# Optimization experiments

Measured on AMD Instinct MI355X. Metric: run time of the kernel, lower is better.

The kernel has to match this reference:

```python
import jax, jax.numpy as jnp
import numpy as np

TIME_STEP = 0.1  # matches module-level time_step in the torch source
STEPS = 65536


def setup_inputs() -> dict:
    key = jax.random.key(0)
    k1, k2 = jax.random.split(key)
    x = jax.random.normal(k1, (12,), dtype=jnp.float32)          # initial state [pos(6), vel(6)]
    actions = jax.random.normal(k2, (STEPS, 6), dtype=jnp.float32)  # learned per-step accelerations
    return {"x": x, "actions": actions}


def reference(x, actions):
    dt = jnp.float32(TIME_STEP)
    half_dt2 = jnp.float32(0.5) * dt * dt

    def step(state, a):
        # state: [12] = [pos(6), vel(6)]; a: [6]
        pos = state[:6] + state[6:] * dt + half_dt2 * a
        vel = state[6:] + dt * a
        new_state = jnp.concatenate([pos, vel])
        return new_state, new_state

    _, states = jax.lax.scan(step, x, actions)  # states: [steps, 12]
    return (states, actions)
```

## Files before the change

### kernel.cpp

```cpp
#include <hip/hip_runtime.h>


#define STEPS   65536
#define NCH     6
#define STATE   12
#define NB      256
#define CHUNK   (STEPS / NB)
#define BLK     (NCH * 64)
#define ACT_OFF (STEPS * STATE)

__device__ double             g_bsum[NB * NCH * 2];
__device__ unsigned long long g_flag[NB * 8];

__global__ __launch_bounds__(BLK) void k_fused(const float4* __restrict__ act4,
                                               const float* __restrict__ x,
                                               float* __restrict__ out) {
    __shared__ float sIn[CHUNK * NCH];
    __shared__ float sOut[CHUNK * STATE];
    __shared__ unsigned long long sEpoch;
    const int b = blockIdx.x, tid = threadIdx.x;

    float4 v = act4[b * (CHUNK * NCH / 4) + tid];
    ((float4*)sIn)[tid] = v;
    __syncthreads();

    const int c = tid >> 6, lane = tid & 63;

    {
        double sA = 0.0, sW = 0.0;
#pragma unroll
        for (int k = 0; k < 4; ++k) {
            const int   tl = k * 64 + lane;
            const float a  = sIn[tl * NCH + c];
            sA += (double)a;
            sW += (double)(b * CHUNK + tl) * (double)a;
        }
#pragma unroll
        for (int off = 32; off > 0; off >>= 1) {
            sA += __shfl_down(sA, off, 64);
            sW += __shfl_down(sW, off, 64);
        }
        if (lane == 0) {
            __hip_atomic_store(&g_bsum[(b * NCH + c) * 2 + 0], sA,
                               __ATOMIC_RELAXED, __HIP_MEMORY_SCOPE_AGENT);
            __hip_atomic_store(&g_bsum[(b * NCH + c) * 2 + 1], sW,
                               __ATOMIC_RELAXED, __HIP_MEMORY_SCOPE_AGENT);
        }
    }

    __syncthreads();
    if (tid == 0) {
        unsigned long long old = __hip_atomic_fetch_add(&g_flag[b * 8], 1ULL,
                                                        __ATOMIC_RELAXED,
                                                        __HIP_MEMORY_SCOPE_AGENT);
        sEpoch = old + 1ULL;
    }
    __syncthreads();
    const unsigned long long e = sEpoch;
    if (tid < 64) {
        unsigned pend = 0xFu;
        for (;;) {
#pragma unroll
            for (int j = 0; j < 4; ++j) {
                if (pend & (1u << j)) {
                    unsigned long long f =
                        __hip_atomic_load(&g_flag[(lane + 64 * j) * 8],
                                          __ATOMIC_RELAXED,
                                          __HIP_MEMORY_SCOPE_AGENT);
                    if (f >= e) pend &= ~(1u << j);
                }
            }
            if (__all(pend == 0u)) break;
            __builtin_amdgcn_s_sleep(1);
        }
        __builtin_amdgcn_fence(__ATOMIC_ACQUIRE, "agent");
    }
    __syncthreads();

    ((float4*)(out + ACT_OFF))[b * (CHUNK * NCH / 4) + tid] = v;

    double offA, offW;
    {
        const double2* bs2 = (const double2*)g_bsum;
        double vA = 0.0, vW = 0.0;
#pragma unroll
        for (int k = 0; k < 4; ++k) {
            const int idx = k * 64 + lane;
            if (idx < b) {
                const double2 p = bs2[idx * NCH + c];
                vA += p.x;
                vW += p.y;
            }
        }
#pragma unroll
        for (int off = 32; off > 0; off >>= 1) {
            vA += __shfl_down(vA, off, 64);
            vW += __shfl_down(vW, off, 64);
        }
        offA = __shfl(vA, 0, 64);
        offW = __shfl(vW, 0, 64);
    }

    const double dt  = (double)0.1f;
    const double dt2 = dt * dt;
    const double p0  = (double)x[c];
    const double v0  = (double)x[NCH + c];

    double accA = offA, accW = offW;
#pragma unroll
    for (int k = 0; k < 4; ++k) {
        const int   tl = k * 64 + lane;
        const int   t  = b * CHUNK + tl;
        const float a  = sIn[tl * NCH + c];
        double iA = (double)a;
        double iW = (double)t * (double)a;
#pragma unroll
        for (int off = 1; off < 64; off <<= 1) {
            const double uA = __shfl_up(iA, off, 64);
            const double uW = __shfl_up(iW, off, 64);
            if (lane >= off) { iA += uA; iW += uW; }
        }
        const double runA = accA + iA;
        const double runW = accW + iW;
        const double vel = v0 + dt * runA;
        const double pos = p0 + dt * (double)(t + 1) * v0
                         + dt2 * (((double)t + 0.5) * runA - runW);
        sOut[tl * STATE + c]       = (float)pos;
        sOut[tl * STATE + NCH + c] = (float)vel;
        accA += __shfl(iA, 63, 64);
        accW += __shfl(iW, 63, 64);
    }
    __syncthreads();

    const float4* so4 = (const float4*)sOut;
    float4*       o4  = (float4*)out;
    o4[b * (CHUNK * STATE / 4) + tid]       = so4[tid];
    o4[b * (CHUNK * STATE / 4) + BLK + tid] = so4[BLK + tid];
}

extern "C" void kernel_launch(void* const* d_in, const int* in_sizes, int n_in,
                              void* d_out, int out_size, void* d_ws, size_t ws_size,
                              hipStream_t stream) {
    const float*  x    = (const float*)d_in[0];
    const float4* act4 = (const float4*)d_in[1];
    float*        out  = (float*)d_out;

    hipLaunchKernelGGL(k_fused, dim3(NB), dim3(BLK), 0, stream,
                       act4, x, out);
}
```

Baseline: 63.74 us.

## Replace all-to-all flag polling with single-block gather and broadcast go flag

Grid barrier now has block 0 alone poll all per-block flags, then publish a single go counter that every other block spins on. Previously each block polled all 256 flags. The intra-chunk scans, the action copy-out and the x loads move ahead of the wait so they overlap with barrier latency. The flag fetch_add becomes a load plus store, and the barrier adds an extra hop through block 0.

```diff
diff --git a/kernel.cpp b/kernel.cpp
--- a/kernel.cpp
+++ b/kernel.cpp
@@ -11,6 +11,7 @@
 
 __device__ double             g_bsum[NB * NCH * 2];
 __device__ unsigned long long g_flag[NB * 8];
+__device__ unsigned long long g_go;
 
 __global__ __launch_bounds__(BLK) void k_fused(const float4* __restrict__ act4,
                                                const float* __restrict__ x,
@@ -19,12 +20,17 @@
     __shared__ float sOut[CHUNK * STATE];
     __shared__ unsigned long long sEpoch;
     const int b = blockIdx.x, tid = threadIdx.x;
+    const int c = tid >> 6, lane = tid & 63;
 
     float4 v = act4[b * (CHUNK * NCH / 4) + tid];
+    const double p0 = (double)x[c];
+    const double v0 = (double)x[NCH + c];
+    unsigned long long myflag = 0ULL;
+    if (tid == 0)
+        myflag = __hip_atomic_load(&g_flag[b * 8], __ATOMIC_RELAXED,
+                                   __HIP_MEMORY_SCOPE_AGENT);
     ((float4*)sIn)[tid] = v;
     __syncthreads();
-
-    const int c = tid >> 6, lane = tid & 63;
 
     {
         double sA = 0.0, sW = 0.0;
@@ -47,17 +53,16 @@
                                __ATOMIC_RELAXED, __HIP_MEMORY_SCOPE_AGENT);
         }
     }
-
-    __syncthreads();
-    if (tid == 0) {
-        unsigned long long old = __hip_atomic_fetch_add(&g_flag[b * 8], 1ULL,
-                                                        __ATOMIC_RELAXED,
-                                                        __HIP_MEMORY_SCOPE_AGENT);
-        sEpoch = old + 1ULL;
-    }
+    if (tid == 0) sEpoch = myflag + 1ULL;
     __syncthreads();
     const unsigned long long e = sEpoch;
-    if (tid < 64) {
+    if (tid == 0)
+        __hip_atomic_store(&g_flag[b * 8], e,
+                           __ATOMIC_RELAXED, __HIP_MEMORY_SCOPE_AGENT);
+
+    ((float4*)(out + ACT_OFF))[b * (CHUNK * NCH / 4) + tid] = v;
+
+    if (b == 0 && tid < 64) {
         unsigned pend = 0xFu;
         for (;;) {
 #pragma unroll
@@ -73,11 +78,38 @@
             if (__all(pend == 0u)) break;
             __builtin_amdgcn_s_sleep(1);
         }
+        if (lane == 0)
+            __hip_atomic_store(&g_go, e,
+                               __ATOMIC_RELAXED, __HIP_MEMORY_SCOPE_AGENT);
+    }
+
+    double iA[4], iW[4], tTotA[4], tTotW[4];
+#pragma unroll
+    for (int k = 0; k < 4; ++k) {
+        const int   tl = k * 64 + lane;
+        const int   t  = b * CHUNK + tl;
+        const float a  = sIn[tl * NCH + c];
+        double a_ = (double)a;
+        double w_ = (double)t * (double)a;
+#pragma unroll
+        for (int off = 1; off < 64; off <<= 1) {
+            const double uA = __shfl_up(a_, off, 64);
+            const double uW = __shfl_up(w_, off, 64);
+            if (lane >= off) { a_ += uA; w_ += uW; }
+        }
+        iA[k] = a_;  iW[k] = w_;
+        tTotA[k] = __shfl(a_, 63, 64);
+        tTotW[k] = __shfl(w_, 63, 64);
+    }
+
+    if (tid < 64) {
+        while (__hip_atomic_load(&g_go, __ATOMIC_RELAXED,
+                                 __HIP_MEMORY_SCOPE_AGENT) < e) {
+            __builtin_amdgcn_s_sleep(1);
+        }
         __builtin_amdgcn_fence(__ATOMIC_ACQUIRE, "agent");
     }
     __syncthreads();
-
-    ((float4*)(out + ACT_OFF))[b * (CHUNK * NCH / 4) + tid] = v;
 
     double offA, offW;
     {
@@ -103,32 +135,20 @@
 
     const double dt  = (double)0.1f;
     const double dt2 = dt * dt;
-    const double p0  = (double)x[c];
-    const double v0  = (double)x[NCH + c];
-
     double accA = offA, accW = offW;
 #pragma unroll
     for (int k = 0; k < 4; ++k) {
-        const int   tl = k * 64 + lane;
-        const int   t  = b * CHUNK + tl;
-        const float a  = sIn[tl * NCH + c];
-        double iA = (double)a;
-        double iW = (double)t * (double)a;
-#pragma unroll
-        for (int off = 1; off < 64; off <<= 1) {
-            const double uA = __shfl_up(iA, off, 64);
-            const double uW = __shfl_up(iW, off, 64);
-            if (lane >= off) { iA += uA; iW += uW; }
-        }
-        const double runA = accA + iA;
-        const double runW = accW + iW;
+        const int tl = k * 64 + lane;
+        const int t  = b * CHUNK + tl;
+        const double runA = accA + iA[k];
+        const double runW = accW + iW[k];
         const double vel = v0 + dt * runA;
         const double pos = p0 + dt * (double)(t + 1) * v0
                          + dt2 * (((double)t + 0.5) * runA - runW);
         sOut[tl * STATE + c]       = (float)pos;
         sOut[tl * STATE + NCH + c] = (float)vel;
-        accA += __shfl(iA, 63, 64);
-        accW += __shfl(iW, 63, 64);
+        accA += tTotA[k];
+        accW += tTotW[k];
     }
     __syncthreads();
 
```

Result: no change. 63.25 us (-0.8%).
